# Performance work log

Hardware: AMD Instinct MI355X
Metric: run time of the kernel (lower is better)

The kernel has to match this reference:

```python
import jax, jax.numpy as jnp
import numpy as np
import math

D_MODEL = 768
NUM_HEADS = 12
D_K = D_MODEL // NUM_HEADS

def setup_inputs() -> dict:
    key = jax.random.key(0)
    k_x, k_q, k_k, k_v, k_o = jax.random.split(key, 5)
    x = jax.random.normal(k_x, (2, 2048, D_MODEL), dtype=jnp.float32)
    std = math.sqrt(2.0 / (D_MODEL + D_MODEL))
    # trunc_normal approx: clip normal to [-3std, 3std]
    def tn(k):
        return jnp.clip(jax.random.normal(k, (D_MODEL, D_MODEL), dtype=jnp.float32) * std, -3 * std, 3 * std)
    return {
        "x": x,
        "weight_query": tn(k_q),
        "weight_key": tn(k_k),
        "weight_value": tn(k_v),
        "weight_output": tn(k_o),
    }

def reference(x, weight_query, weight_key, weight_value, weight_output):
    # x: (b, s, d_model); weights: (d_out, d_model)
    b, s, _ = x.shape
    def proj_heads(w):
        y = jnp.einsum('od,bsd->bso', w, x)  # (b, s, h*dk)
        return y.reshape(b, s, NUM_HEADS, D_K).transpose(0, 2, 1, 3)  # (b, h, s, dk)
    Q = proj_heads(weight_query)
    K = proj_heads(weight_key)
    V = proj_heads(weight_value)
    scores = jnp.einsum('bhqd,bhkd->bhqk', Q, K) / jnp.sqrt(jnp.asarray(D_K, x.dtype))
    causal = jnp.tril(jnp.ones((s, s), dtype=bool))  # (sq, sk)
    scores = jnp.where(causal, scores, -jnp.inf)
    attn = jax.nn.softmax(scores, axis=-1)
    out_heads = jnp.einsum('bhqk,bhkd->bhqd', attn, V)  # (b, h, s, dv)
    attn_out = out_heads.transpose(0, 2, 1, 3).reshape(b, s, NUM_HEADS * D_K)
    return jnp.einsum('di,bsi->bsd', weight_output, attn_out)
```

## Files before the change

### kernel.cpp

```cpp
#include <hip/hip_runtime.h>
#include <stdint.h>

typedef float f32x4 __attribute__((ext_vector_type(4)));
typedef __bf16 bf16x8 __attribute__((ext_vector_type(8)));
typedef uint32_t u32a  __attribute__((may_alias));
typedef uint2    u2a   __attribute__((may_alias));
typedef uint4    u4a   __attribute__((may_alias));

#define VS 2064

__device__ __forceinline__ ushort f2b(float f) {
  uint32_t u = __builtin_bit_cast(uint32_t, f);
  u += 0x7FFFu + ((u >> 16) & 1u);
  return (ushort)(u >> 16);
}
__device__ __forceinline__ uint32_t b16(uint32_t u) {
  u += 0x7FFFu + ((u >> 16) & 1u);
  return u >> 16;
}

__device__ __forceinline__ bf16x8 ld_frag(const ushort* p) {
  u4a u = *(const u4a*)p;
  return __builtin_bit_cast(bf16x8, u);
}

__device__ __forceinline__ u4a cvt8(const float* p) {
  u4a a = *(const u4a*)p, b = *(const u4a*)(p + 4), o;
  o.x = b16(a.x) | (b16(a.y) << 16);
  o.y = b16(a.z) | (b16(a.w) << 16);
  o.z = b16(b.x) | (b16(b.y) << 16);
  o.w = b16(b.z) | (b16(b.w) << 16);
  return o;
}

__device__ __forceinline__ void load_lds16(const void* g, void* l) {
  __builtin_amdgcn_global_load_lds(
      (const __attribute__((address_space(1))) uint32_t*)g,
      (__attribute__((address_space(3))) uint32_t*)l, 16, 0, 0);
}

__device__ __forceinline__ uint32_t comb2(uint32_t a, uint32_t b, float w0, float w1) {
  float lo = __builtin_bit_cast(float, a << 16) * w0 +
             __builtin_bit_cast(float, b << 16) * w1;
  float hi = __builtin_bit_cast(float, a & 0xFFFF0000u) * w0 +
             __builtin_bit_cast(float, b & 0xFFFF0000u) * w1;
  return (uint32_t)f2b(lo) | ((uint32_t)f2b(hi) << 16);
}

__global__ __launch_bounds__(256) void convert_kernel(
    const float* __restrict__ x,  const float* __restrict__ wq,
    const float* __restrict__ wk, const float* __restrict__ wv,
    const float* __restrict__ wo,
    ushort* __restrict__ xb,  ushort* __restrict__ wqb,
    ushort* __restrict__ wkb, ushort* __restrict__ wvb,
    ushort* __restrict__ wob)
{
  const size_t NX = 3145728, NW = 589824;
  size_t idx = ((size_t)blockIdx.x * 256 + threadIdx.x) * 8;
  const float* src; ushort* dst; size_t off;
  if      (idx < NX)          { src = x;  dst = xb;  off = idx; }
  else if (idx < NX + NW)     { src = wq; dst = wqb; off = idx - NX; }
  else if (idx < NX + 2 * NW) { src = wk; dst = wkb; off = idx - NX - NW; }
  else if (idx < NX + 3 * NW) { src = wv; dst = wvb; off = idx - NX - 2 * NW; }
  else                        { src = wo; dst = wob; off = idx - NX - 3 * NW; }
  *(u4a*)(dst + off) = cvt8(src + off);
}

__global__ __launch_bounds__(256) void gemm_qkv(
    const ushort* __restrict__ A,
    const ushort* __restrict__ B0, const ushort* __restrict__ B1,
    const ushort* __restrict__ B2,
    ushort* __restrict__ Qo, ushort* __restrict__ Ko, ushort* __restrict__ Vt,
    int M, int N, int K)
{
  const ushort* B = blockIdx.z == 0 ? B0 : (blockIdx.z == 1 ? B1 : B2);
  const int m0 = blockIdx.x * 128, n0 = blockIdx.y * 64;
  __shared__ ushort As[128 * 32];
  __shared__ ushort Bs[64 * 32];
  const int tid = threadIdx.x, wave = tid >> 6, lane = tid & 63;
  const int quad = lane >> 4, l16 = lane & 15;
  const int mw = (wave & 1) * 64, nw = (wave >> 1) * 32;
  f32x4 acc[4][2] = {};

  for (int k0 = 0; k0 < K; k0 += 32) {
#pragma unroll
    for (int i = 0; i < 2; ++i) {
      int c = i * 256 + tid;
      load_lds16(A + (size_t)(m0 + (c >> 2)) * K + k0 + (c & 3) * 8,
                 As + (size_t)(i * 256 + wave * 64) * 8);
    }
    load_lds16(B + (size_t)(n0 + (tid >> 2)) * K + k0 + (tid & 3) * 8,
               Bs + (size_t)(wave * 64) * 8);
    __syncthreads();
    bf16x8 af[4], bfr[2];
#pragma unroll
    for (int i = 0; i < 4; ++i) af[i]  = ld_frag(As + (mw + i * 16 + l16) * 32 + quad * 8);
#pragma unroll
    for (int j = 0; j < 2; ++j) bfr[j] = ld_frag(Bs + (nw + j * 16 + l16) * 32 + quad * 8);
#pragma unroll
    for (int i = 0; i < 4; ++i)
#pragma unroll
      for (int j = 0; j < 2; ++j)
        acc[i][j] = __builtin_amdgcn_mfma_f32_16x16x32_bf16(af[i], bfr[j], acc[i][j], 0, 0, 0);
    __syncthreads();
  }
  if (blockIdx.z < 2) {
    ushort* C = blockIdx.z == 0 ? Qo : Ko;
#pragma unroll
    for (int i = 0; i < 4; ++i)
#pragma unroll
      for (int j = 0; j < 2; ++j)
#pragma unroll
        for (int r = 0; r < 4; ++r) {
          int row = m0 + mw + i * 16 + quad * 4 + r;
          int col = n0 + nw + j * 16 + l16;
          C[(size_t)row * N + col] = f2b(acc[i][j][r]);
        }
  } else {
#pragma unroll
    for (int i = 0; i < 4; ++i)
#pragma unroll
      for (int j = 0; j < 2; ++j) {
        int col = n0 + nw + j * 16 + l16;
        int h = col >> 6, dv = col & 63;
        int t = m0 + mw + i * 16 + quad * 4;
        int b = t >> 11, s = t & 2047;
        u2a pw;
        pw.x = (uint32_t)f2b(acc[i][j][0]) | ((uint32_t)f2b(acc[i][j][1]) << 16);
        pw.y = (uint32_t)f2b(acc[i][j][2]) | ((uint32_t)f2b(acc[i][j][3]) << 16);
        *(u2a*)(Vt + (((size_t)b * 12 + h) * 64 + dv) * VS + s) = pw;
      }
  }
}

__global__ __launch_bounds__(256) void gemm_out(
    const ushort* __restrict__ A, const ushort* __restrict__ B,
    float* __restrict__ C, int M, int N, int K)
{
  const int m0 = blockIdx.x * 64, n0 = blockIdx.y * 64;
  __shared__ ushort As[64 * 32];
  __shared__ ushort Bs[64 * 32];
  const int tid = threadIdx.x, wave = tid >> 6, lane = tid & 63;
  const int quad = lane >> 4, l16 = lane & 15;
  const int mw = (wave & 1) * 32, nw = (wave >> 1) * 32;
  f32x4 acc[2][2] = {};

  for (int k0 = 0; k0 < K; k0 += 32) {
    load_lds16(A + (size_t)(m0 + (tid >> 2)) * K + k0 + (tid & 3) * 8,
               As + (size_t)(wave * 64) * 8);
    load_lds16(B + (size_t)(n0 + (tid >> 2)) * K + k0 + (tid & 3) * 8,
               Bs + (size_t)(wave * 64) * 8);
    __syncthreads();
    bf16x8 af[2], bfr[2];
#pragma unroll
    for (int i = 0; i < 2; ++i) af[i]  = ld_frag(As + (mw + i * 16 + l16) * 32 + quad * 8);
#pragma unroll
    for (int j = 0; j < 2; ++j) bfr[j] = ld_frag(Bs + (nw + j * 16 + l16) * 32 + quad * 8);
#pragma unroll
    for (int i = 0; i < 2; ++i)
#pragma unroll
      for (int j = 0; j < 2; ++j)
        acc[i][j] = __builtin_amdgcn_mfma_f32_16x16x32_bf16(af[i], bfr[j], acc[i][j], 0, 0, 0);
    __syncthreads();
  }
#pragma unroll
  for (int i = 0; i < 2; ++i)
#pragma unroll
    for (int j = 0; j < 2; ++j)
#pragma unroll
      for (int r = 0; r < 4; ++r) {
        int row = m0 + mw + i * 16 + quad * 4 + r;
        int col = n0 + nw + j * 16 + l16;
        C[(size_t)row * N + col] = acc[i][j][r];
      }
}

__global__ __launch_bounds__(256) void attn_kernel(
    const ushort* __restrict__ Qb, const ushort* __restrict__ Kb,
    const ushort* __restrict__ Vt, ushort* __restrict__ Opart,
    float2* __restrict__ MLp)
{
  const int S = 2048, DM = 768;
  const int pair = blockIdx.x >> 1, j = blockIdx.x & 1;
  const int h = blockIdx.y, bb = blockIdx.z;
  const ushort* Qp  = Qb + (size_t)bb * S * DM + h * 64;
  const ushort* Kp  = Kb + (size_t)bb * S * DM + h * 64;
  const ushort* Vth = Vt + ((size_t)bb * 12 + h) * 64 * VS;

  __shared__ ushort Ks[128 * 72];
  __shared__ ushort Vs[64 * 136];
  __shared__ ushort Ps[4][16 * 136];

  const int tid = threadIdx.x, wave = tid >> 6, lane = tid & 63;
  const int quad = lane >> 4, l16 = lane & 15;
  const float LOG2E = 1.44269504f;
  const float NEG_BIG = -1.0e30f;

  for (int sp = 0; sp < 2; ++sp) {
    const int qt = sp == 0 ? pair : 31 - pair;
    const int q0 = qt * 64;
    const int qg = q0 + wave * 16 + l16;

    bf16x8 bq0 = ld_frag(Qp + (size_t)qg * DM + quad * 8);
    bf16x8 bq1 = ld_frag(Qp + (size_t)qg * DM + 32 + quad * 8);

    f32x4 acc_o[4] = {};
    float m_run = NEG_BIG, l_run = 0.0f;
    const int nkt = (qt >> 1) + 1;

    for (int kt = j; kt < nkt; kt += 2) {
      const int kk0 = kt * 128;
#pragma unroll
      for (int i = 0; i < 4; ++i) {
        int c = i * 256 + tid;
        int r = c >> 3, col = (c & 7) * 8;
        *(u4a*)(Ks + r * 72 + col) = *(const u4a*)(Kp + (size_t)(kk0 + r) * DM + col);
      }
#pragma unroll
      for (int i = 0; i < 4; ++i) {
        int c = i * 256 + tid;
        int dv = c >> 4, kc = (c & 15) * 8;
        *(u4a*)(Vs + dv * 136 + kc) = *(const u4a*)(Vth + (size_t)dv * VS + kk0 + kc);
      }
      __syncthreads();

      f32x4 sacc[8] = {};
#pragma unroll
      for (int tt = 0; tt < 8; ++tt) {
        bf16x8 ak0 = ld_frag(Ks + (tt * 16 + l16) * 72 + quad * 8);
        bf16x8 ak1 = ld_frag(Ks + (tt * 16 + l16) * 72 + 32 + quad * 8);
        sacc[tt] = __builtin_amdgcn_mfma_f32_16x16x32_bf16(ak0, bq0, sacc[tt], 0, 0, 0);
        sacc[tt] = __builtin_amdgcn_mfma_f32_16x16x32_bf16(ak1, bq1, sacc[tt], 0, 0, 0);
      }

      const bool domask = (kt == nkt - 1);
      float sv[8][4];
      float mt = NEG_BIG;
#pragma unroll
      for (int tt = 0; tt < 8; ++tt)
#pragma unroll
        for (int r = 0; r < 4; ++r) {
          float s = sacc[tt][r] * 0.125f;
          if (domask) {
            int kkg = kk0 + tt * 16 + quad * 4 + r;
            if (kkg > qg) s = NEG_BIG;
          }
          sv[tt][r] = s;
          mt = fmaxf(mt, s);
        }
      mt = fmaxf(mt, __shfl_xor(mt, 16, 64));
      mt = fmaxf(mt, __shfl_xor(mt, 32, 64));
      float mnew = fmaxf(m_run, mt);
      float alpha = exp2f((m_run - mnew) * LOG2E);
      float lsum = 0.0f;
#pragma unroll
      for (int tt = 0; tt < 8; ++tt) {
        float p0 = exp2f((sv[tt][0] - mnew) * LOG2E);
        float p1 = exp2f((sv[tt][1] - mnew) * LOG2E);
        float p2 = exp2f((sv[tt][2] - mnew) * LOG2E);
        float p3 = exp2f((sv[tt][3] - mnew) * LOG2E);
        lsum += (p0 + p1) + (p2 + p3);
        u2a pw;
        pw.x = (uint32_t)f2b(p0) | ((uint32_t)f2b(p1) << 16);
        pw.y = (uint32_t)f2b(p2) | ((uint32_t)f2b(p3) << 16);
        *(u2a*)(&Ps[wave][l16 * 136 + tt * 16 + quad * 4]) = pw;
      }
      asm volatile("s_waitcnt lgkmcnt(0)" ::: "memory");
      lsum += __shfl_xor(lsum, 16, 64);
      lsum += __shfl_xor(lsum, 32, 64);
      l_run = l_run * alpha + lsum;
      m_run = mnew;

      float ar0 = __shfl(alpha, quad * 4 + 0, 64);
      float ar1 = __shfl(alpha, quad * 4 + 1, 64);
      float ar2 = __shfl(alpha, quad * 4 + 2, 64);
      float ar3 = __shfl(alpha, quad * 4 + 3, 64);
#pragma unroll
      for (int ct = 0; ct < 4; ++ct) {
        acc_o[ct][0] *= ar0; acc_o[ct][1] *= ar1;
        acc_o[ct][2] *= ar2; acc_o[ct][3] *= ar3;
      }

#pragma unroll
      for (int ks = 0; ks < 4; ++ks) {
        bf16x8 ap = ld_frag(&Ps[wave][l16 * 136 + ks * 32 + quad * 8]);
#pragma unroll
        for (int ct = 0; ct < 4; ++ct) {
          bf16x8 bv = ld_frag(Vs + (size_t)(ct * 16 + l16) * 136 + ks * 32 + quad * 8);
          acc_o[ct] = __builtin_amdgcn_mfma_f32_16x16x32_bf16(ap, bv, acc_o[ct], 0, 0, 0);
        }
      }
      __syncthreads();
    }

    const int slot = (((bb * 12 + h) << 5) + qt) * 2 + j;
    ushort* Os = Opart + (size_t)slot * 4096;
    const int r0 = wave * 16 + quad * 4;
#pragma unroll
    for (int ct = 0; ct < 4; ++ct) {
      int col = ct * 16 + l16;
      Os[(r0 + 0) * 64 + col] = f2b(acc_o[ct][0]);
      Os[(r0 + 1) * 64 + col] = f2b(acc_o[ct][1]);
      Os[(r0 + 2) * 64 + col] = f2b(acc_o[ct][2]);
      Os[(r0 + 3) * 64 + col] = f2b(acc_o[ct][3]);
    }
    if (quad == 0)
      MLp[(size_t)slot * 64 + wave * 16 + l16] = make_float2(m_run, l_run);
  }
}

__global__ __launch_bounds__(256) void combine_kernel(
    const ushort* __restrict__ Opart, const float2* __restrict__ MLp,
    ushort* __restrict__ Ab)
{
  const int sid = blockIdx.x;
  const int bb = sid / 384, rem = sid % 384, h = rem >> 5, qt = rem & 31;
  const int t = threadIdx.x, row = t >> 2, cg = (t & 3) * 16;
  float2 ml0 = MLp[(size_t)(sid * 2) * 64 + row];
  float2 ml1 = MLp[(size_t)(sid * 2 + 1) * 64 + row];
  float ms = fmaxf(ml0.x, ml1.x);
  float w0 = exp2f((ml0.x - ms) * 1.44269504f);
  float w1 = exp2f((ml1.x - ms) * 1.44269504f);
  float inv = 1.0f / (ml0.y * w0 + ml1.y * w1);
  w0 *= inv; w1 *= inv;
  const ushort* p0 = Opart + (size_t)(sid * 2) * 4096 + row * 64 + cg;
  ushort* dst = Ab + ((size_t)(bb * 2048 + qt * 64 + row)) * 768 + h * 64 + cg;
#pragma unroll
  for (int g = 0; g < 2; ++g) {
    u4a a = *(const u4a*)(p0 + g * 8);
    u4a b = *(const u4a*)(p0 + 4096 + g * 8);
    u4a o;
    o.x = comb2(a.x, b.x, w0, w1);
    o.y = comb2(a.y, b.y, w0, w1);
    o.z = comb2(a.z, b.z, w0, w1);
    o.w = comb2(a.w, b.w, w0, w1);
    *(u4a*)(dst + g * 8) = o;
  }
}

extern "C" void kernel_launch(void* const* d_in, const int* in_sizes, int n_in,
                              void* d_out, int out_size, void* d_ws, size_t ws_size,
                              hipStream_t stream) {
  (void)in_sizes; (void)n_in; (void)out_size; (void)ws_size;
  const float* x  = (const float*)d_in[0];
  const float* wq = (const float*)d_in[1];
  const float* wk = (const float*)d_in[2];
  const float* wv = (const float*)d_in[3];
  const float* wo = (const float*)d_in[4];

  const size_t NT = (size_t)4096 * 768;
  const size_t NW = (size_t)768 * 768;
  const size_t NV = (size_t)24 * 64 * VS;
  ushort* xb    = (ushort*)d_ws;
  ushort* Qbuf  = xb + NT;
  ushort* Kbuf  = Qbuf + NT;
  ushort* Vt    = Kbuf + NT;
  ushort* wqb   = Vt + NV;
  ushort* wkb   = wqb + NW;
  ushort* wvb   = wkb + NW;
  ushort* wob   = wvb + NW;
  ushort* Opart = wob + NW;
  float2* MLp   = (float2*)(Opart + (size_t)1536 * 4096);
  ushort* Abuf  = xb;

  convert_kernel<<<2688, 256, 0, stream>>>(x, wq, wk, wv, wo,
                                           xb, wqb, wkb, wvb, wob);
  gemm_qkv<<<dim3(32, 12, 3), 256, 0, stream>>>(
      xb, wqb, wkb, wvb, Qbuf, Kbuf, Vt, 4096, 768, 768);
  attn_kernel<<<dim3(32, 12, 2), 256, 0, stream>>>(Qbuf, Kbuf, Vt, Opart, MLp);
  combine_kernel<<<768, 256, 0, stream>>>(Opart, MLp, Abuf);
  gemm_out<<<dim3(64, 12), 256, 0, stream>>>(
      Abuf, wob, (float*)d_out, 4096, 768, 768);
}
```

Before: 175.3 us.

## Read V fragments directly from global memory, fold score scale into Q, truncate P

```diff
diff --git a/kernel.cpp b/kernel.cpp
--- a/kernel.cpp
+++ b/kernel.cpp
@@ -106,6 +106,7 @@
   }
   if (blockIdx.z < 2) {
     ushort* C = blockIdx.z == 0 ? Qo : Ko;
+    const float sc = blockIdx.z == 0 ? 0.125f : 1.0f;
 #pragma unroll
     for (int i = 0; i < 4; ++i)
 #pragma unroll
@@ -114,7 +115,7 @@
         for (int r = 0; r < 4; ++r) {
           int row = m0 + mw + i * 16 + quad * 4 + r;
           int col = n0 + nw + j * 16 + l16;
-          C[(size_t)row * N + col] = f2b(acc[i][j][r]);
+          C[(size_t)row * N + col] = f2b(acc[i][j][r] * sc);
         }
   } else {
 #pragma unroll
@@ -188,7 +189,6 @@
   const ushort* Vth = Vt + ((size_t)bb * 12 + h) * 64 * VS;
 
   __shared__ ushort Ks[128 * 72];
-  __shared__ ushort Vs[64 * 136];
   __shared__ ushort Ps[4][16 * 136];
 
   const int tid = threadIdx.x, wave = tid >> 6, lane = tid & 63;
@@ -215,12 +215,6 @@
         int c = i * 256 + tid;
         int r = c >> 3, col = (c & 7) * 8;
         *(u4a*)(Ks + r * 72 + col) = *(const u4a*)(Kp + (size_t)(kk0 + r) * DM + col);
-      }
-#pragma unroll
-      for (int i = 0; i < 4; ++i) {
-        int c = i * 256 + tid;
-        int dv = c >> 4, kc = (c & 15) * 8;
-        *(u4a*)(Vs + dv * 136 + kc) = *(const u4a*)(Vth + (size_t)dv * VS + kk0 + kc);
       }
       __syncthreads();
 
@@ -234,18 +228,17 @@
       }
 
       const bool domask = (kt == nkt - 1);
-      float sv[8][4];
       float mt = NEG_BIG;
 #pragma unroll
       for (int tt = 0; tt < 8; ++tt)
 #pragma unroll
         for (int r = 0; r < 4; ++r) {
-          float s = sacc[tt][r] * 0.125f;
+          float s = sacc[tt][r];
           if (domask) {
             int kkg = kk0 + tt * 16 + quad * 4 + r;
             if (kkg > qg) s = NEG_BIG;
           }
-          sv[tt][r] = s;
+          sacc[tt][r] = s;
           mt = fmaxf(mt, s);
         }
       mt = fmaxf(mt, __shfl_xor(mt, 16, 64));
@@ -255,14 +248,18 @@
       float lsum = 0.0f;
 #pragma unroll
       for (int tt = 0; tt < 8; ++tt) {
-        float p0 = exp2f((sv[tt][0] - mnew) * LOG2E);
-        float p1 = exp2f((sv[tt][1] - mnew) * LOG2E);
-        float p2 = exp2f((sv[tt][2] - mnew) * LOG2E);
-        float p3 = exp2f((sv[tt][3] - mnew) * LOG2E);
+        float p0 = exp2f((sacc[tt][0] - mnew) * LOG2E);
+        float p1 = exp2f((sacc[tt][1] - mnew) * LOG2E);
+        float p2 = exp2f((sacc[tt][2] - mnew) * LOG2E);
+        float p3 = exp2f((sacc[tt][3] - mnew) * LOG2E);
         lsum += (p0 + p1) + (p2 + p3);
+        uint32_t u0 = __builtin_bit_cast(uint32_t, p0);
+        uint32_t u1 = __builtin_bit_cast(uint32_t, p1);
+        uint32_t u2 = __builtin_bit_cast(uint32_t, p2);
+        uint32_t u3 = __builtin_bit_cast(uint32_t, p3);
         u2a pw;
-        pw.x = (uint32_t)f2b(p0) | ((uint32_t)f2b(p1) << 16);
-        pw.y = (uint32_t)f2b(p2) | ((uint32_t)f2b(p3) << 16);
+        pw.x = (u0 >> 16) | (u1 & 0xFFFF0000u);
+        pw.y = (u2 >> 16) | (u3 & 0xFFFF0000u);
         *(u2a*)(&Ps[wave][l16 * 136 + tt * 16 + quad * 4]) = pw;
       }
       asm volatile("s_waitcnt lgkmcnt(0)" ::: "memory");
@@ -281,12 +278,13 @@
         acc_o[ct][2] *= ar2; acc_o[ct][3] *= ar3;
       }
 
+      const ushort* vb = Vth + kk0;
 #pragma unroll
       for (int ks = 0; ks < 4; ++ks) {
         bf16x8 ap = ld_frag(&Ps[wave][l16 * 136 + ks * 32 + quad * 8]);
 #pragma unroll
         for (int ct = 0; ct < 4; ++ct) {
-          bf16x8 bv = ld_frag(Vs + (size_t)(ct * 16 + l16) * 136 + ks * 32 + quad * 8);
+          bf16x8 bv = ld_frag(vb + (size_t)(ct * 16 + l16) * VS + ks * 32 + quad * 8);
           acc_o[ct] = __builtin_amdgcn_mfma_f32_16x16x32_bf16(ap, bv, acc_o[ct], 0, 0, 0);
         }
       }
```

Result: slower. 199.4 us (+13.7%).
